# Kernel optimization log

Hardware: AMD Instinct MI355X
Metric: run time of the kernel (lower is better)

## Reference

```python
import jax, jax.numpy as jnp
import numpy as np

N_NODES = 50000
N_EDGES = 800000
D_IN = 256
D_OUT = 128
EPS = 1e-9


def setup_inputs() -> dict:
    key = jax.random.key(0)
    ks = jax.random.split(key, 6)
    feat = jax.random.normal(ks[0], (N_NODES, D_IN), dtype=jnp.float32)
    edge_row = jax.random.randint(ks[1], (N_EDGES,), 0, N_NODES)
    edge_col = jax.random.randint(ks[2], (N_EDGES,), 0, N_NODES)
    # normalized adjacency values (positive, ~1/degree scale)
    edge_val = jax.random.uniform(ks[3], (N_EDGES,), dtype=jnp.float32) / 16.0
    # xavier_uniform for Linear(dim_in, dim_out) weights, stored as [D_IN, D_OUT]
    limit = float(np.sqrt(6.0 / (D_IN + D_OUT)))
    W0 = jax.random.uniform(ks[4], (D_IN, D_OUT), minval=-limit, maxval=limit, dtype=jnp.float32)
    W1 = jax.random.uniform(ks[5], (D_IN, D_OUT), minval=-limit, maxval=limit, dtype=jnp.float32)
    zeros = jnp.zeros((D_OUT,), dtype=jnp.float32)
    ones = jnp.ones((D_OUT,), dtype=jnp.float32)
    return {
        "feat": feat,
        "W0": W0, "b0": zeros, "scale0": ones, "offset0": zeros,
        "W1": W1, "b1": zeros, "scale1": ones, "offset1": zeros,
        "edge_row": edge_row, "edge_col": edge_col, "edge_val": edge_val,
    }


def _spmm(edge_row, edge_col, edge_val, x):
    # out[r] += val * x[c] for each edge (r, c, val)  -- sparse adj @ x
    msgs = edge_val[:, None] * x[edge_col]  # [E, D]
    return jax.ops.segment_sum(msgs, edge_row, num_segments=N_NODES)


def _feat_trans(x, W, b, scale, offset):
    h = jax.nn.relu(x @ W + b)  # [N, D_OUT]
    mean = jnp.mean(h, axis=1, keepdims=True)
    var = jnp.var(h, axis=1, keepdims=True) + EPS  # unbiased=False (population var)
    return (h - mean) * scale * jax.lax.rsqrt(var) + offset


def reference(feat, W0, b0, scale0, offset0, W1, b1, scale1, offset1,
              edge_row, edge_col, edge_val):
    # non-first-layer path: feat_hop = [X, A @ X] (order=1), dropout p=0 is identity
    hop1 = _spmm(edge_row, edge_col, edge_val, feat)
    f0 = _feat_trans(feat, W0, b0, scale0, offset0)
    f1 = _feat_trans(hop1, W1, b1, scale1, offset1)
    return jnp.concatenate([f0, f1], axis=1)  # aggr == 'concat'
```

## Files before the change

### kernel.cpp

```cpp
#include <hip/hip_runtime.h>

#define N_NODES 50000
#define N_EDGES 800000
#define D_IN    256
#define D_OUT   128
#define EPS     1e-9f
#define BSTR    72

#define SCATTER_BLOCKS 196
#define GEMM_MBLKS     391

#define RPB    64
#define NBUCK  782
#define BCAP   1344
#define GSTR   16
#define LCAP   1792

#define SORT_OFF  0
#define HIST_OFF  32768
#define LOFF_OFF  35896
#define BASE_OFF  39024
#define CSUM_OFF  42152
#define CBAS_OFF  42216
#define SMEM_BYTES 42280

typedef __attribute__((ext_vector_type(8))) short bf16x8;
typedef __attribute__((ext_vector_type(4))) float floatx4;

__device__ __forceinline__ ushort f2bf(float x) {
    unsigned u = __float_as_uint(x);
    u += 0x7fffu + ((u >> 16) & 1u);
    return (ushort)(u >> 16);
}

__device__ __forceinline__ bf16x8 packbf(float4 a, float4 b) {
    union { ushort us[8]; bf16x8 v; } r;
    r.us[0] = f2bf(a.x); r.us[1] = f2bf(a.y);
    r.us[2] = f2bf(a.z); r.us[3] = f2bf(a.w);
    r.us[4] = f2bf(b.x); r.us[5] = f2bf(b.y);
    r.us[6] = f2bf(b.z); r.us[7] = f2bf(b.w);
    return r.v;
}

#define WB_BLOCKS  32
__global__ __launch_bounds__(256) void prep_small(
    const float* __restrict__ W0, const float* __restrict__ W1,
    ushort* __restrict__ Wb, int* __restrict__ gcnt)
{
    int bid = blockIdx.x;
    int t   = threadIdx.x;
    if (bid == 0) {
        for (int i = t; i < NBUCK * GSTR; i += 256) gcnt[i] = 0;
    } else {
        int g  = (bid - 1) * 256 + t;
        int n  = g >> 5;
        int kq = g & 31;
        const float* W = (n < 128) ? W0 : W1;
        int nn = n & 127;
        union { ushort us[8]; uint4 v; } tmp;
#pragma unroll
        for (int j = 0; j < 8; ++j)
            tmp.us[j] = f2bf(W[(size_t)(kq * 8 + j) * D_OUT + nn]);
        *(uint4*)&Wb[(size_t)n * D_IN + kq * 8] = tmp.v;
    }
}

__global__ __launch_bounds__(512, 4) void gemm_scatter(
    const float* __restrict__ feat, const ushort* __restrict__ Wb,
    const float* __restrict__ bias, const float* __restrict__ scale,
    const float* __restrict__ offset,
    float* __restrict__ out, ushort* __restrict__ Y1,
    const int* __restrict__ er, const int* __restrict__ ec,
    const float* __restrict__ ev, int* __restrict__ gcnt,
    uint2* __restrict__ bedge)
{
    __shared__ __align__(16) char smem[SMEM_BYTES];

    const int t = threadIdx.x;

    if (blockIdx.x < SCATTER_BLOCKS) {
        uint2* sorted = (uint2*)(smem + SORT_OFF);
        int*   hist   = (int*)(smem + HIST_OFF);
        int*   loff   = (int*)(smem + LOFF_OFF);
        int*   base   = (int*)(smem + BASE_OFF);
        int*   csum   = (int*)(smem + CSUM_OFF);
        int*   cbas   = (int*)(smem + CBAS_OFF);

        for (int i = t; i < NBUCK; i += 512) hist[i] = 0;
        __syncthreads();

        const int ebase  = blockIdx.x * 4096;
        const int ecount = min(4096, N_EDGES - ebase);
        int   bkt[8], rnk[8];
        uint2 pk[8];
#pragma unroll
        for (int u = 0; u < 8; ++u) {
            int e = ebase + u * 512 + t;
            bool ok = (e < N_EDGES);
            int   r = ok ? er[e] : 0;
            int   c = ok ? ec[e] : 0;
            float v = ok ? ev[e] : 0.f;
            int   b = r >> 6;
            bkt[u] = ok ? b : -1;
            pk[u]  = make_uint2(((unsigned)b << 22) |
                                ((unsigned)(r & 63) << 16) | (unsigned)c,
                                __float_as_uint(v));
            if (ok) rnk[u] = atomicAdd(&hist[b], 1);
        }
        __syncthreads();

        {
            const int lane = t & 63, w = t >> 6;
            int v0 = (t < NBUCK) ? hist[t] : 0;
            int x0 = v0;
#pragma unroll
            for (int s = 1; s < 64; s <<= 1) {
                int y = __shfl_up(x0, s);
                if (lane >= s) x0 += y;
            }
            if (lane == 63) csum[w] = x0;
            const int i1 = t + 512;
            int v1 = (i1 < NBUCK) ? hist[i1] : 0;
            int x1 = v1;
#pragma unroll
            for (int s = 1; s < 64; s <<= 1) {
                int y = __shfl_up(x1, s);
                if (lane >= s) x1 += y;
            }
            if (lane == 63) csum[8 + w] = x1;
            __syncthreads();
            if (t == 0) {
                int run = 0;
#pragma unroll
                for (int c = 0; c < 16; ++c) { cbas[c] = run; run += csum[c]; }
            }
            __syncthreads();
            if (t < NBUCK)  loff[t]  = x0 - v0 + cbas[w];
            if (i1 < NBUCK) loff[i1] = x1 - v1 + cbas[8 + w];
        }
        __syncthreads();

#pragma unroll
        for (int u = 0; u < 8; ++u) {
            if (bkt[u] >= 0)
                sorted[loff[bkt[u]] + rnk[u]] = pk[u];
        }
        for (int i = t; i < NBUCK; i += 512) {
            int h = hist[i];
            base[i] = h ? atomicAdd(&gcnt[i * GSTR], h) : 0;
        }
        __syncthreads();

#pragma unroll
        for (int u = 0; u < 8; ++u) {
            int k = t + u * 512;
            if (k < ecount) {
                uint2 e = sorted[k];
                int b   = (int)(e.x >> 22);
                int pos = base[b] + (k - loff[b]);
                if (pos < BCAP)
                    bedge[(size_t)b * BCAP + pos] = e;
            }
        }
        return;
    }

    const int mblk = blockIdx.x - SCATTER_BLOCKS;
    const int wave = t >> 6, lane = t & 63;
    const int quad = lane >> 4, l16 = lane & 15;
    const int m0   = mblk * 128;
    ushort* Bs = (ushort*)smem;

    const int grow = m0 + wave * 16 + l16;
    const int arow = grow < N_NODES ? grow : 0;
    const float* aptr = &feat[(size_t)arow * D_IN + quad * 8];

    floatx4 acc[16];
#pragma unroll
    for (int nt = 0; nt < 16; ++nt)
        acc[nt] = (floatx4){0.f, 0.f, 0.f, 0.f};

    for (int kt = 0; kt < D_IN; kt += 64) {
#pragma unroll
        for (int i = 0; i < 4; ++i) {
            int g = t + i * 512;
            int row = g >> 3, kq = g & 7;
            *(uint4*)&Bs[row * BSTR + kq * 8] =
                *(const uint4*)&Wb[(size_t)row * D_IN + kt + kq * 8];
        }
        __syncthreads();

        const float* p = aptr + kt;
        float4 q0 = *(const float4*)(p +  0), q1 = *(const float4*)(p +  4);
        float4 q2 = *(const float4*)(p + 32), q3 = *(const float4*)(p + 36);
        bf16x8 a0 = packbf(q0, q1), a1 = packbf(q2, q3);

#pragma unroll
        for (int s = 0; s < 2; ++s) {
            bf16x8 a = s ? a1 : a0;
            const int kk = s * 32;
            bf16x8 b[8];
#pragma unroll
            for (int nt = 0; nt < 8; ++nt)
                b[nt] = *(bf16x8*)&Bs[(nt * 16 + l16) * BSTR + kk + quad * 8];
#pragma unroll
            for (int nt = 0; nt < 8; ++nt)
                acc[nt] = __builtin_amdgcn_mfma_f32_16x16x32_bf16(
                    a, b[nt], acc[nt], 0, 0, 0);
#pragma unroll
            for (int nt = 0; nt < 8; ++nt)
                b[nt] = *(bf16x8*)&Bs[(128 + nt * 16 + l16) * BSTR + kk + quad * 8];
#pragma unroll
            for (int nt = 0; nt < 8; ++nt)
                acc[8 + nt] = __builtin_amdgcn_mfma_f32_16x16x32_bf16(
                    a, b[nt], acc[8 + nt], 0, 0, 0);
        }
        __syncthreads();
    }

    {
        float bb[8], sc[8], of[8];
#pragma unroll
        for (int nt = 0; nt < 8; ++nt) {
            bb[nt] = bias[nt * 16 + l16];
            sc[nt] = scale[nt * 16 + l16];
            of[nt] = offset[nt * 16 + l16];
        }
#pragma unroll
        for (int i = 0; i < 4; ++i) {
            float h[8], s = 0.f, q = 0.f;
#pragma unroll
            for (int nt = 0; nt < 8; ++nt) {
                h[nt] = fmaxf(acc[nt][i] + bb[nt], 0.f);
                s += h[nt];
                q += h[nt] * h[nt];
            }
#pragma unroll
            for (int m = 1; m < 16; m <<= 1) {
                s += __shfl_xor(s, m);
                q += __shfl_xor(q, m);
            }
            float mean = s * (1.f / 128.f);
            float inv  = rsqrtf(q * (1.f / 128.f) - mean * mean + EPS);
            int row = m0 + wave * 16 + quad * 4 + i;
            if (row < N_NODES) {
#pragma unroll
                for (int nt = 0; nt < 8; ++nt)
                    out[(size_t)row * 256 + nt * 16 + l16] =
                        (h[nt] - mean) * sc[nt] * inv + of[nt];
#pragma unroll
                for (int nt = 0; nt < 8; ++nt)
                    Y1[(size_t)row * D_OUT + nt * 16 + l16] =
                        f2bf(acc[8 + nt][i]);
            }
        }
    }
}

__global__ __launch_bounds__(512) void spmm_csr_ln(
    const int* __restrict__ gcnt, const uint2* __restrict__ bedge,
    const ushort* __restrict__ Y,
    const float* __restrict__ bias, const float* __restrict__ scale,
    const float* __restrict__ offset, float* __restrict__ out)
{
    __shared__ uint2 lds_e[LCAP];
    __shared__ int   cnt[RPB];
    __shared__ int   offx[RPB];
    __shared__ int   cntp[RPB];

    const int t      = threadIdx.x;
    const int bucket = blockIdx.x;
    const int r0     = bucket * RPB;
    const int nrows  = min(RPB, N_NODES - r0);
    int ne = gcnt[bucket * GSTR];
    ne = ne < BCAP ? ne : BCAP;

    if (t < RPB) cnt[t] = 0;
    {
        uint4* ez = (uint4*)lds_e;
        ez[t] = make_uint4(0u, 0u, 0u, 0u);
        if (t + 512 < 896) ez[t + 512] = make_uint4(0u, 0u, 0u, 0u);
    }
    __syncthreads();

    const size_t base = (size_t)bucket * BCAP;
    int   erA = -1, erB = -1, erC = -1;
    unsigned exA = 0, exB = 0, exC = 0;
    unsigned evA = 0, evB = 0, evC = 0;
    int   rkA = 0,  rkB = 0,  rkC = 0;
    if (t < ne) {
        uint2 p = bedge[base + t];
        erA = (int)((p.x >> 16) & 63u); exA = (p.x & 0xffffu) << 8;
        evA = p.y;
        rkA = atomicAdd(&cnt[erA], 1);
    }
    if (t + 512 < ne) {
        uint2 p = bedge[base + t + 512];
        erB = (int)((p.x >> 16) & 63u); exB = (p.x & 0xffffu) << 8;
        evB = p.y;
        rkB = atomicAdd(&cnt[erB], 1);
    }
    if (t + 1024 < ne) {
        uint2 p = bedge[base + t + 1024];
        erC = (int)((p.x >> 16) & 63u); exC = (p.x & 0xffffu) << 8;
        evC = p.y;
        rkC = atomicAdd(&cnt[erC], 1);
    }
    __syncthreads();

    if (t < RPB) {
        int c  = cnt[t];
        int cp = (c + 7) & ~7;
        int x  = cp;
#pragma unroll
        for (int s = 1; s < RPB; s <<= 1) {
            int w = __shfl_up(x, s);
            if (t >= s) x += w;
        }
        offx[t] = x - cp;
        cntp[t] = cp;
    }
    __syncthreads();

    if (erA >= 0) lds_e[offx[erA] + rkA] = make_uint2(exA, evA);
    if (erB >= 0) lds_e[offx[erB] + rkB] = make_uint2(exB, evB);
    if (erC >= 0) lds_e[offx[erC] + rkC] = make_uint2(exC, evC);
    __syncthreads();

    const int wave  = t >> 6, lane = t & 63;
    const int lane4 = lane * 4;
    const int cidx  = lane * 2;
    const char* Yb  = (const char*)Y;
    const float b0v = bias[cidx],   b1v = bias[cidx + 1];
    const float s0v = scale[cidx],  s1v = scale[cidx + 1];
    const float o0v = offset[cidx], o1v = offset[cidx + 1];

    for (int ri = wave; ri < nrows; ri += 8) {
        int beg = offx[ri], np = cntp[ri];
        float ax = 0.f, ay = 0.f;
        for (int j = 0; j < np; j += 8) {
            uint2 e[8];
#pragma unroll
            for (int u = 0; u < 8; ++u)
                e[u] = lds_e[beg + j + u];
            unsigned yv[8];
#pragma unroll
            for (int u = 0; u < 8; ++u)
                yv[u] = *(const unsigned*)(Yb + e[u].x + lane4);
#pragma unroll
            for (int u = 0; u < 8; ++u) {
                float v = __uint_as_float(e[u].y);
                ax = fmaf(v, __uint_as_float(yv[u] << 16), ax);
                ay = fmaf(v, __uint_as_float(yv[u] & 0xffff0000u), ay);
            }
        }
        float h0 = fmaxf(ax + b0v, 0.f);
        float h1 = fmaxf(ay + b1v, 0.f);
        float s = h0 + h1, q = h0 * h0 + h1 * h1;
#pragma unroll
        for (int m = 1; m < 64; m <<= 1) {
            s += __shfl_xor(s, m);
            q += __shfl_xor(q, m);
        }
        float mean = s * (1.f / 128.f);
        float inv  = rsqrtf(q * (1.f / 128.f) - mean * mean + EPS);
        int row = r0 + ri;
        float2 o;
        o.x = (h0 - mean) * s0v * inv + o0v;
        o.y = (h1 - mean) * s1v * inv + o1v;
        *(float2*)&out[(size_t)row * 256 + 128 + cidx] = o;
    }
}

extern "C" void kernel_launch(void* const* d_in, const int* in_sizes, int n_in,
                              void* d_out, int out_size, void* d_ws, size_t ws_size,
                              hipStream_t stream)
{
    const float* feat = (const float*)d_in[0];
    const float* W0   = (const float*)d_in[1];
    const float* b0   = (const float*)d_in[2];
    const float* s0   = (const float*)d_in[3];
    const float* o0   = (const float*)d_in[4];
    const float* W1   = (const float*)d_in[5];
    const float* b1   = (const float*)d_in[6];
    const float* s1   = (const float*)d_in[7];
    const float* o1   = (const float*)d_in[8];
    const int*   er   = (const int*)d_in[9];
    const int*   ec   = (const int*)d_in[10];
    const float* ev   = (const float*)d_in[11];
    float* out = (float*)d_out;

    char*   wsb   = (char*)d_ws;
    ushort* Wb    = (ushort*)(wsb);
    ushort* Y1    = (ushort*)(wsb + 131072);
    int*    gcnt  = (int*)   (wsb + 12931072);
    uint2*  bedge = (uint2*) (wsb + 12981248);

    prep_small<<<1 + WB_BLOCKS, 256, 0, stream>>>(W0, W1, Wb, gcnt);

    gemm_scatter<<<SCATTER_BLOCKS + GEMM_MBLKS, 512, 0, stream>>>(
        feat, Wb, b0, s0, o0, out, Y1, er, ec, ev, gcnt, bedge);

    spmm_csr_ln<<<NBUCK, 512, 0, stream>>>(
        gcnt, bedge, Y1, b1, s1, o1, out);
}
```

Measured before the change: 178.5 us.

## Split fused scatter/GEMM kernel and preload full A row before K loop

The combined gemm_scatter kernel, whose block index chose between edge bucketing and the dense GEMM, becomes two kernels, edge_scatter and gemm_ln, launched back to back on the same stream. Each kernel now sizes its own shared memory, so the GEMM no longer reserves the scatter's larger footprint. The GEMM also loads all 256 input features for its row up front and converts them to bf16 once, instead of loading a 64-wide slice each K step, which lets global loads issue ahead of the MFMA loop. The cost is an extra kernel launch, no overlap between scatter and GEMM blocks, and higher register pressure from holding eight bf16x8 A fragments.

```diff
diff --git a/kernel.cpp b/kernel.cpp
--- a/kernel.cpp
+++ b/kernel.cpp
@@ -15,14 +15,6 @@
 #define BCAP   1344
 #define GSTR   16
 #define LCAP   1792
-
-#define SORT_OFF  0
-#define HIST_OFF  32768
-#define LOFF_OFF  35896
-#define BASE_OFF  39024
-#define CSUM_OFF  42152
-#define CBAS_OFF  42216
-#define SMEM_BYTES 42280
 
 typedef __attribute__((ext_vector_type(8))) short bf16x8;
 typedef __attribute__((ext_vector_type(4))) float floatx4;
@@ -65,122 +57,138 @@
     }
 }
 
-__global__ __launch_bounds__(512, 4) void gemm_scatter(
-    const float* __restrict__ feat, const ushort* __restrict__ Wb,
-    const float* __restrict__ bias, const float* __restrict__ scale,
-    const float* __restrict__ offset,
-    float* __restrict__ out, ushort* __restrict__ Y1,
+__global__ __launch_bounds__(512) void edge_scatter(
     const int* __restrict__ er, const int* __restrict__ ec,
     const float* __restrict__ ev, int* __restrict__ gcnt,
     uint2* __restrict__ bedge)
 {
-    __shared__ __align__(16) char smem[SMEM_BYTES];
+    __shared__ uint2 sorted[4096];
+    __shared__ int   hist[NBUCK];
+    __shared__ int   loff[NBUCK];
+    __shared__ int   base[NBUCK];
+    __shared__ int   csum[16];
+    __shared__ int   cbas[16];
 
     const int t = threadIdx.x;
 
-    if (blockIdx.x < SCATTER_BLOCKS) {
-        uint2* sorted = (uint2*)(smem + SORT_OFF);
-        int*   hist   = (int*)(smem + HIST_OFF);
-        int*   loff   = (int*)(smem + LOFF_OFF);
-        int*   base   = (int*)(smem + BASE_OFF);
-        int*   csum   = (int*)(smem + CSUM_OFF);
-        int*   cbas   = (int*)(smem + CBAS_OFF);
-
-        for (int i = t; i < NBUCK; i += 512) hist[i] = 0;
+    for (int i = t; i < NBUCK; i += 512) hist[i] = 0;
+    __syncthreads();
+
+    const int ebase  = blockIdx.x * 4096;
+    const int ecount = min(4096, N_EDGES - ebase);
+    int   bkt[8], rnk[8];
+    uint2 pk[8];
+#pragma unroll
+    for (int u = 0; u < 8; ++u) {
+        int e = ebase + u * 512 + t;
+        bool ok = (e < N_EDGES);
+        int   r = ok ? er[e] : 0;
+        int   c = ok ? ec[e] : 0;
+        float v = ok ? ev[e] : 0.f;
+        int   b = r >> 6;
+        bkt[u] = ok ? b : -1;
+        pk[u]  = make_uint2(((unsigned)b << 22) |
+                            ((unsigned)(r & 63) << 16) | (unsigned)c,
+                            __float_as_uint(v));
+        if (ok) rnk[u] = atomicAdd(&hist[b], 1);
+    }
+    __syncthreads();
+
+    {
+        const int lane = t & 63, w = t >> 6;
+        int v0 = (t < NBUCK) ? hist[t] : 0;
+        int x0 = v0;
+#pragma unroll
+        for (int s = 1; s < 64; s <<= 1) {
+            int y = __shfl_up(x0, s);
+            if (lane >= s) x0 += y;
+        }
+        if (lane == 63) csum[w] = x0;
+        const int i1 = t + 512;
+        int v1 = (i1 < NBUCK) ? hist[i1] : 0;
+        int x1 = v1;
+#pragma unroll
+        for (int s = 1; s < 64; s <<= 1) {
+            int y = __shfl_up(x1, s);
+            if (lane >= s) x1 += y;
+        }
+        if (lane == 63) csum[8 + w] = x1;
         __syncthreads();
-
-        const int ebase  = blockIdx.x * 4096;
-        const int ecount = min(4096, N_EDGES - ebase);
-        int   bkt[8], rnk[8];
-        uint2 pk[8];
-#pragma unroll
-        for (int u = 0; u < 8; ++u) {
-            int e = ebase + u * 512 + t;
-            bool ok = (e < N_EDGES);
-            int   r = ok ? er[e] : 0;
-            int   c = ok ? ec[e] : 0;
-            float v = ok ? ev[e] : 0.f;
-            int   b = r >> 6;
-            bkt[u] = ok ? b : -1;
-            pk[u]  = make_uint2(((unsigned)b << 22) |
-                                ((unsigned)(r & 63) << 16) | (unsigned)c,
-                                __float_as_uint(v));
-            if (ok) rnk[u] = atomicAdd(&hist[b], 1);
+        if (t == 0) {
+            int run = 0;
+#pragma unroll
+            for (int c = 0; c < 16; ++c) { cbas[c] = run; run += csum[c]; }
         }
         __syncthreads();
-
-        {
-            const int lane = t & 63, w = t >> 6;
-            int v0 = (t < NBUCK) ? hist[t] : 0;
-            int x0 = v0;
-#pragma unroll
-            for (int s = 1; s < 64; s <<= 1) {
-                int y = __shfl_up(x0, s);
-                if (lane >= s) x0 += y;
-            }
-            if (lane == 63) csum[w] = x0;
-            const int i1 = t + 512;
-            int v1 = (i1 < NBUCK) ? hist[i1] : 0;
-            int x1 = v1;
-#pragma unroll
-            for (int s = 1; s < 64; s <<= 1) {
-                int y = __shfl_up(x1, s);
-                if (lane >= s) x1 += y;
-            }
-            if (lane == 63) csum[8 + w] = x1;
-            __syncthreads();
-            if (t == 0) {
-                int run = 0;
-#pragma unroll
-                for (int c = 0; c < 16; ++c) { cbas[c] = run; run += csum[c]; }
-            }
-            __syncthreads();
-            if (t < NBUCK)  loff[t]  = x0 - v0 + cbas[w];
-            if (i1 < NBUCK) loff[i1] = x1 - v1 + cbas[8 + w];
-        }
-        __syncthreads();
-
-#pragma unroll
-        for (int u = 0; u < 8; ++u) {
-            if (bkt[u] >= 0)
-                sorted[loff[bkt[u]] + rnk[u]] = pk[u];
-        }
-        for (int i = t; i < NBUCK; i += 512) {
-            int h = hist[i];
-            base[i] = h ? atomicAdd(&gcnt[i * GSTR], h) : 0;
-        }
-        __syncthreads();
-
-#pragma unroll
-        for (int u = 0; u < 8; ++u) {
-            int k = t + u * 512;
-            if (k < ecount) {
-                uint2 e = sorted[k];
-                int b   = (int)(e.x >> 22);
-                int pos = base[b] + (k - loff[b]);
-                if (pos < BCAP)
-                    bedge[(size_t)b * BCAP + pos] = e;
-            }
-        }
-        return;
-    }
-
-    const int mblk = blockIdx.x - SCATTER_BLOCKS;
+        if (t < NBUCK)  loff[t]  = x0 - v0 + cbas[w];
+        if (i1 < NBUCK) loff[i1] = x1 - v1 + cbas[8 + w];
+    }
+    __syncthreads();
+
+#pragma unroll
+    for (int u = 0; u < 8; ++u) {
+        if (bkt[u] >= 0)
+            sorted[loff[bkt[u]] + rnk[u]] = pk[u];
+    }
+    for (int i = t; i < NBUCK; i += 512) {
+        int h = hist[i];
+        base[i] = h ? atomicAdd(&gcnt[i * GSTR], h) : 0;
+    }
+    __syncthreads();
+
+#pragma unroll
+    for (int u = 0; u < 8; ++u) {
+        int k = t + u * 512;
+        if (k < ecount) {
+            uint2 e = sorted[k];
+            int b   = (int)(e.x >> 22);
+            int pos = base[b] + (k - loff[b]);
+            if (pos < BCAP)
+                bedge[(size_t)b * BCAP + pos] = e;
+        }
+    }
+}
+
+__global__ __launch_bounds__(512, 4) void gemm_ln(
+    const float* __restrict__ feat, const ushort* __restrict__ Wb,
+    const float* __restrict__ bias, const float* __restrict__ scale,
+    const float* __restrict__ offset,
+    float* __restrict__ out, ushort* __restrict__ Y1)
+{
+    __shared__ __align__(16) ushort Bs[256 * BSTR];
+
+    const int t    = threadIdx.x;
+    const int mblk = blockIdx.x;
     const int wave = t >> 6, lane = t & 63;
     const int quad = lane >> 4, l16 = lane & 15;
     const int m0   = mblk * 128;
-    ushort* Bs = (ushort*)smem;
 
     const int grow = m0 + wave * 16 + l16;
     const int arow = grow < N_NODES ? grow : 0;
-    const float* aptr = &feat[(size_t)arow * D_IN + quad * 8];
+    const float* p = &feat[(size_t)arow * D_IN + quad * 8];
+
+    float4 w0 = *(const float4*)(p +   0), w1 = *(const float4*)(p +   4);
+    float4 w2 = *(const float4*)(p +  32), w3 = *(const float4*)(p +  36);
+    float4 w4 = *(const float4*)(p +  64), w5 = *(const float4*)(p +  68);
+    float4 w6 = *(const float4*)(p +  96), w7 = *(const float4*)(p + 100);
+    float4 w8 = *(const float4*)(p + 128), w9 = *(const float4*)(p + 132);
+    float4 wA = *(const float4*)(p + 160), wB = *(const float4*)(p + 164);
+    float4 wC = *(const float4*)(p + 192), wD = *(const float4*)(p + 196);
+    float4 wE = *(const float4*)(p + 224), wF = *(const float4*)(p + 228);
+    bf16x8 a[8];
+    a[0] = packbf(w0, w1); a[1] = packbf(w2, w3);
+    a[2] = packbf(w4, w5); a[3] = packbf(w6, w7);
+    a[4] = packbf(w8, w9); a[5] = packbf(wA, wB);
+    a[6] = packbf(wC, wD); a[7] = packbf(wE, wF);
 
     floatx4 acc[16];
 #pragma unroll
     for (int nt = 0; nt < 16; ++nt)
         acc[nt] = (floatx4){0.f, 0.f, 0.f, 0.f};
 
-    for (int kt = 0; kt < D_IN; kt += 64) {
+#pragma unroll
+    for (int ph = 0; ph < 4; ++ph) {
+        const int kt = ph * 64;
 #pragma unroll
         for (int i = 0; i < 4; ++i) {
             int g = t + i * 512;
@@ -190,14 +198,9 @@
         }
         __syncthreads();
 
-        const float* p = aptr + kt;
-        float4 q0 = *(const float4*)(p +  0), q1 = *(const float4*)(p +  4);
-        float4 q2 = *(const float4*)(p + 32), q3 = *(const float4*)(p + 36);
-        bf16x8 a0 = packbf(q0, q1), a1 = packbf(q2, q3);
-
 #pragma unroll
         for (int s = 0; s < 2; ++s) {
-            bf16x8 a = s ? a1 : a0;
+            bf16x8 av = a[ph * 2 + s];
             const int kk = s * 32;
             bf16x8 b[8];
 #pragma unroll
@@ -206,14 +209,14 @@
 #pragma unroll
             for (int nt = 0; nt < 8; ++nt)
                 acc[nt] = __builtin_amdgcn_mfma_f32_16x16x32_bf16(
-                    a, b[nt], acc[nt], 0, 0, 0);
+                    av, b[nt], acc[nt], 0, 0, 0);
 #pragma unroll
             for (int nt = 0; nt < 8; ++nt)
                 b[nt] = *(bf16x8*)&Bs[(128 + nt * 16 + l16) * BSTR + kk + quad * 8];
 #pragma unroll
             for (int nt = 0; nt < 8; ++nt)
                 acc[8 + nt] = __builtin_amdgcn_mfma_f32_16x16x32_bf16(
-                    a, b[nt], acc[8 + nt], 0, 0, 0);
+                    av, b[nt], acc[8 + nt], 0, 0, 0);
         }
         __syncthreads();
     }
@@ -398,8 +401,9 @@
 
     prep_small<<<1 + WB_BLOCKS, 256, 0, stream>>>(W0, W1, Wb, gcnt);
 
-    gemm_scatter<<<SCATTER_BLOCKS + GEMM_MBLKS, 512, 0, stream>>>(
-        feat, Wb, b0, s0, o0, out, Y1, er, ec, ev, gcnt, bedge);
+    edge_scatter<<<SCATTER_BLOCKS, 512, 0, stream>>>(er, ec, ev, gcnt, bedge);
+
+    gemm_ln<<<GEMM_MBLKS, 512, 0, stream>>>(feat, Wb, b0, s0, o0, out, Y1);
 
     spmm_csr_ln<<<NBUCK, 512, 0, stream>>>(
         gcnt, bedge, Y1, b1, s1, o1, out);
```

Measured after the change: 187.0 us. +4.8%, slower.
